# Performance work log

Measured on AMD Instinct MI355X. Metric: run time of the kernel, lower is better.

## Reference

```python
import jax, jax.numpy as jnp
import numpy as np

H = 512          # hidden_size
B, S, L = 32, 2048, 2
D = 2 * H        # encoder output / hidden feature dim


def setup_inputs() -> dict:
    key = jax.random.key(0)
    ks = jax.random.split(key, 9)
    lim1 = 1.0 / np.sqrt(D)
    limv = 1.0 / np.sqrt(H)
    return {
        "hidden": jax.random.normal(ks[0], (L, B, D), jnp.float32),
        "encoder_outputs": jax.random.normal(ks[1], (B, S, D), jnp.float32),
        "mask": jax.random.randint(ks[2], (B, S), 0, 2, jnp.int32),
        "W1_w": jax.random.uniform(ks[3], (H, D), jnp.float32, -lim1, lim1),
        "W1_b": jax.random.uniform(ks[4], (H,), jnp.float32, -lim1, lim1),
        "W2_w": jax.random.uniform(ks[5], (H, D), jnp.float32, -lim1, lim1),
        "W2_b": jax.random.uniform(ks[6], (H,), jnp.float32, -lim1, lim1),
        "V_w": jax.random.uniform(ks[7], (1, H), jnp.float32, -limv, limv),
        "V_b": jax.random.uniform(ks[8], (1,), jnp.float32, -limv, limv),
    }


def reference(hidden, encoder_outputs, mask, W1_w, W1_b, W2_w, W2_b, V_w, V_b):
    # query: last layer hidden state, broadcast over sequence -> [B, 1, D]
    query = hidden[-1][:, None, :]
    # W1(enc) + W2(query): [B, S, H]
    proj = (jnp.einsum('bsd,hd->bsh', encoder_outputs, W1_w) + W1_b
            + jnp.einsum('bqd,hd->bqh', query, W2_w) + W2_b)
    # V projection -> scores [B, S]
    score = jnp.einsum('bsh,h->bs', jnp.tanh(proj), V_w[0]) + V_b[0]
    score = jnp.where(mask == 0, jnp.float32(-1e9), score)
    attn_weights = jax.nn.softmax(score, axis=1)          # [B, S]
    context = jnp.einsum('bs,bsd->bd', attn_weights, encoder_outputs)  # [B, D]
    return context, attn_weights
```

## Files before the change

kernel.cpp:

```cpp
#include <hip/hip_runtime.h>
#include <hip/hip_bf16.h>

#define B_ 32
#define S_ 2048
#define D_ 1024
#define H_ 512
#define M_ (B_*S_)
#define BM 128
#define BN 128
#define BK 64
#define TILE (BM*BK)

typedef __attribute__((ext_vector_type(8))) short short8;
typedef __attribute__((ext_vector_type(4))) float f32x4;

__device__ __forceinline__ unsigned short f2bf(float f){
  return __builtin_bit_cast(unsigned short, __float2bfloat16(f));
}

__device__ __forceinline__ float fast_tanh(float x){
  return 1.f - 2.f*__builtin_amdgcn_rcpf(__expf(2.f*x) + 1.f);
}

__device__ __forceinline__ int swz(int row, int kshort){
  return row*BK + ((kshort & 56) ^ ((row&7)<<3)) + (kshort & 7);
}

__global__ __launch_bounds__(256) void convw_kernel(
    const float* __restrict__ W1, unsigned short* __restrict__ W1f){
  int g = blockIdx.x*256 + threadIdx.x;
  int lane = g & 63, r = g >> 6;
  int kh = r & 1, ni = (r>>1)&3, wh = (r>>3)&1, kt = (r>>4)&15, bn = r>>8;
  int h  = bn*128 + wh*64 + ni*16 + (lane&15);
  int k0 = kt*64 + kh*32 + (lane>>4)*8;
  const float* src = W1 + (size_t)h*D_ + k0;
  float4 lo = *(const float4*)src;
  float4 hi = *(const float4*)(src+4);
  short8 v;
  v[0]=(short)f2bf(lo.x); v[1]=(short)f2bf(lo.y); v[2]=(short)f2bf(lo.z); v[3]=(short)f2bf(lo.w);
  v[4]=(short)f2bf(hi.x); v[5]=(short)f2bf(hi.y); v[6]=(short)f2bf(hi.z); v[7]=(short)f2bf(hi.w);
  *(short8*)&W1f[(size_t)g*8] = v;
}

__global__ __launch_bounds__(256) void qbias_kernel(
    const float* __restrict__ hidden, const float* __restrict__ W2,
    const float* __restrict__ W1b, const float* __restrict__ W2b,
    float* __restrict__ qb){
  int b = blockIdx.x, h0 = blockIdx.y*64;
  int wave = threadIdx.x>>6, lane = threadIdx.x&63;
  const float* q = hidden + (size_t)(B_ + b)*D_;
  for (int i=0;i<16;i++){
    int h = h0 + wave*16 + i;
    const float* w = W2 + (size_t)h*D_;
    float s = 0.f;
    #pragma unroll
    for (int it=0; it<4; ++it){
      int d = it*256 + lane*4;
      const float4 qq = *(const float4*)(q+d);
      const float4 ww = *(const float4*)(w+d);
      s += qq.x*ww.x + qq.y*ww.y + qq.z*ww.z + qq.w*ww.w;
    }
    #pragma unroll
    for (int off=1; off<64; off<<=1) s += __shfl_xor(s, off);
    if (lane==0) qb[b*H_ + h] = s + W1b[h] + W2b[h];
  }
}

__global__ __launch_bounds__(256, 2) void score_gemm(
    const float* __restrict__ enc, const unsigned short* __restrict__ W1f,
    const float* __restrict__ qb, const float* __restrict__ Vw,
    float* __restrict__ score_p){
  const int id  = blockIdx.x;
  const int xcd = id & 7;
  const int j   = id >> 3;
  const int bm  = xcd*64 + (j >> 2);
  const int bn  = j & 3;
  const int m0 = bm*BM, h0 = bn*BN;
  const int tid = threadIdx.x, lane = tid&63, wave = tid>>6;
  const int wm = (wave>>1)*64, wh = wave&1, wn = wh*64;

  __shared__ __align__(16) unsigned short As[2][TILE];

  f32x4 acc[4][4];
  #pragma unroll
  for (int i=0;i<4;i++)
    #pragma unroll
    for (int j2=0;j2<4;j2++)
      acc[i][j2] = (f32x4)(0.f);

  float4 aLo[4], aHi[4];
  short8 b0[4][2], b1[4][2];

#define LOAD_A(KT) do{ const int kkx=(KT)*BK; \
  _Pragma("unroll") for (int i=0;i<4;i++){ \
    int c=tid+i*256; int row=c>>3, kc=(c&7)*8; \
    const float4* pa=(const float4*)(enc+(size_t)(m0+row)*D_+kkx+kc); \
    aLo[i]=pa[0]; aHi[i]=pa[1]; } }while(0)

#define CVT_A(P) do{ \
  _Pragma("unroll") for (int i=0;i<4;i++){ \
    int c=tid+i*256; int row=c>>3, kc=(c&7)*8; short8 av; \
    av[0]=(short)f2bf(aLo[i].x); av[1]=(short)f2bf(aLo[i].y); \
    av[2]=(short)f2bf(aLo[i].z); av[3]=(short)f2bf(aLo[i].w); \
    av[4]=(short)f2bf(aHi[i].x); av[5]=(short)f2bf(aHi[i].y); \
    av[6]=(short)f2bf(aHi[i].z); av[7]=(short)f2bf(aHi[i].w); \
    *(short8*)&As[P][swz(row,kc)] = av; } }while(0)

#define GLOB_B(KT, BB) do{ \
  const size_t sb = (size_t)(((bn*16+(KT))*2+wh)*8)*512 + lane*8; \
  _Pragma("unroll") for (int ni=0;ni<4;ni++) \
    _Pragma("unroll") for (int kh=0;kh<2;kh++) \
      BB[ni][kh] = *(const short8*)&W1f[sb + (size_t)(ni*2+kh)*512]; }while(0)

#define COMPUTE(P, BB) do{ \
  _Pragma("unroll") for (int kh=0; kh<2; ++kh){ \
    const int kb = kh*32 + (lane>>4)*8; \
    short8 af[4]; \
    _Pragma("unroll") for (int mi=0;mi<4;mi++){ \
      int row=wm+mi*16+(lane&15); af[mi]=*(const short8*)&As[P][swz(row,kb)]; } \
    _Pragma("unroll") for (int mi=0;mi<4;mi++) \
      _Pragma("unroll") for (int ni=0;ni<4;ni++) \
        acc[mi][ni]=__builtin_amdgcn_mfma_f32_16x16x32_bf16(af[mi],BB[ni][kh],acc[mi][ni],0,0,0); \
  } }while(0)

#define BODY(KT, BC, BN_) do{ \
  GLOB_B((KT)+1, BN_); \
  __builtin_amdgcn_sched_barrier(0); \
  COMPUTE((KT)&1, BC); \
  CVT_A(((KT)+1)&1); \
  LOAD_A((KT)+2); \
  asm volatile("s_waitcnt lgkmcnt(0)" ::: "memory"); \
  __builtin_amdgcn_s_barrier(); }while(0)

  LOAD_A(0);
  GLOB_B(0, b0);
  CVT_A(0);
  LOAD_A(1);
  asm volatile("s_waitcnt lgkmcnt(0)" ::: "memory");
  __builtin_amdgcn_s_barrier();

  for (int k2=0; k2<7; ++k2){
    BODY(2*k2,   b0, b1);
    BODY(2*k2+1, b1, b0);
  }
  GLOB_B(15, b1);
  __builtin_amdgcn_sched_barrier(0);
  COMPUTE(0, b0);
  CVT_A(1);
  asm volatile("s_waitcnt lgkmcnt(0)" ::: "memory");
  __builtin_amdgcn_s_barrier();
  COMPUTE(1, b1);

  const int bidx = m0 >> 11;
  float qv[4], vwv[4];
  #pragma unroll
  for (int ni=0;ni<4;ni++){
    int h = h0 + wn + ni*16 + (lane&15);
    qv[ni]  = qb[bidx*H_ + h];
    vwv[ni] = Vw[h];
  }
  __shared__ float psum[4][BM];
  #pragma unroll
  for (int mi=0;mi<4;mi++){
    #pragma unroll
    for (int r=0;r<4;r++){
      float s = 0.f;
      #pragma unroll
      for (int ni=0;ni<4;ni++) s += fast_tanh(acc[mi][ni][r] + qv[ni]) * vwv[ni];
      s += __shfl_xor(s,1); s += __shfl_xor(s,2);
      s += __shfl_xor(s,4); s += __shfl_xor(s,8);
      if ((lane&15)==0){
        int m = wm + mi*16 + ((lane>>4)<<2) + r;
        psum[wave][m] = s;
      }
    }
  }
  __syncthreads();
  if (tid < BM){
    int w0 = (tid>>6)*2;
    score_p[(size_t)bn*M_ + m0 + tid] = psum[w0][tid] + psum[w0+1][tid];
  }
}

__global__ __launch_bounds__(256) void softmax_kernel(
    const float* __restrict__ score_p, const int* __restrict__ mask,
    float* __restrict__ attn){
  int b = blockIdx.x, tid = threadIdx.x;
  int wave = tid>>6, lane = tid&63;
  __shared__ float red[8];
  float v[8];
  float mx = -1e30f;
  #pragma unroll
  for (int i=0;i<8;i++){
    int idx = b*S_ + tid + i*256;
    float sc = score_p[idx] + score_p[M_+idx] + score_p[2*M_+idx] + score_p[3*M_+idx];
    v[i] = (mask[idx]==0) ? -1e9f : sc;
    mx = fmaxf(mx, v[i]);
  }
  #pragma unroll
  for (int off=1; off<64; off<<=1) mx = fmaxf(mx, __shfl_xor(mx, off));
  if (lane==0) red[wave] = mx;
  __syncthreads();
  mx = fmaxf(fmaxf(red[0],red[1]), fmaxf(red[2],red[3]));
  float sum = 0.f;
  #pragma unroll
  for (int i=0;i<8;i++){ v[i] = __expf(v[i]-mx); sum += v[i]; }
  #pragma unroll
  for (int off=1; off<64; off<<=1) sum += __shfl_xor(sum, off);
  if (lane==0) red[4+wave] = sum;
  __syncthreads();
  float inv = 1.f/(red[4]+red[5]+red[6]+red[7]);
  #pragma unroll
  for (int i=0;i<8;i++) attn[b*S_ + tid + i*256] = v[i]*inv;
}

__global__ __launch_bounds__(256) void context_kernel(
    const float* __restrict__ enc, const float* __restrict__ attn,
    float* __restrict__ ctx){
  int b = blockIdx.x, sc = blockIdx.y;
  int s0 = sc*64;
  int d4 = threadIdx.x*4;
  const float* ep = enc + ((size_t)b*S_ + s0)*D_ + d4;
  const float* ap = attn + b*S_ + s0;
  float4 a0 = make_float4(0.f,0.f,0.f,0.f);
  float4 a1 = make_float4(0.f,0.f,0.f,0.f);
  #pragma unroll 4
  for (int i=0;i<64;i+=2){
    float w0 = ap[i], w1 = ap[i+1];
    float4 e0 = *(const float4*)(ep + (size_t)i*D_);
    float4 e1 = *(const float4*)(ep + (size_t)(i+1)*D_);
    a0.x = fmaf(w0, e0.x, a0.x); a0.y = fmaf(w0, e0.y, a0.y);
    a0.z = fmaf(w0, e0.z, a0.z); a0.w = fmaf(w0, e0.w, a0.w);
    a1.x = fmaf(w1, e1.x, a1.x); a1.y = fmaf(w1, e1.y, a1.y);
    a1.z = fmaf(w1, e1.z, a1.z); a1.w = fmaf(w1, e1.w, a1.w);
  }
  float* o = ctx + b*D_ + d4;
  atomicAdd(o+0, a0.x+a1.x); atomicAdd(o+1, a0.y+a1.y);
  atomicAdd(o+2, a0.z+a1.z); atomicAdd(o+3, a0.w+a1.w);
}

extern "C" void kernel_launch(void* const* d_in, const int* in_sizes, int n_in,
                              void* d_out, int out_size, void* d_ws, size_t ws_size,
                              hipStream_t stream){
  const float* hidden = (const float*)d_in[0];
  const float* enc    = (const float*)d_in[1];
  const int*   mask   = (const int*)d_in[2];
  const float* W1w    = (const float*)d_in[3];
  const float* W1b    = (const float*)d_in[4];
  const float* W2w    = (const float*)d_in[5];
  const float* W2b    = (const float*)d_in[6];
  const float* Vw     = (const float*)d_in[7];
  float* out = (float*)d_out;

  float* qb           = (float*)d_ws;
  float* score_p      = qb + B_*H_;
  unsigned short* W1f = (unsigned short*)(score_p + 4*M_);

  hipMemsetAsync(out, 0, (size_t)B_*D_*sizeof(float), stream);

  convw_kernel  <<<H_*D_/8/256,     256, 0, stream>>>(W1w, W1f);
  qbias_kernel  <<<dim3(B_, H_/64), 256, 0, stream>>>(hidden, W2w, W1b, W2b, qb);
  score_gemm    <<<4*(M_/BM),       256, 0, stream>>>(enc, W1f, qb, Vw, score_p);
  softmax_kernel<<<B_,              256, 0, stream>>>(score_p, mask, out + B_*D_);
  context_kernel<<<dim3(B_, 32),    256, 0, stream>>>(enc, out + B_*D_, out);
}
```

Before: 192.8 us.

## Load encoder A fragments directly from global into registers, drop LDS staging

Replaces the shared-memory double-buffered A tile (fp32 load, bf16 convert, swizzled LDS store, barrier, LDS read) with per-wave direct global loads of the exact MFMA A-fragment rows, converted to bf16 in registers. Removes LDS traffic and block barriers, and raises the occupancy hint to 3 blocks per CU. The trade-off is that the two waves sharing the same rows now each read those encoder rows from global memory, doubling A traffic through L2. The loads also come out as less coalesced strided float4 reads, with only half a K-tile of prefetch to hide latency.

```diff
diff --git a/kernel.cpp b/kernel.cpp
--- a/kernel.cpp
+++ b/kernel.cpp
@@ -9,7 +9,6 @@
 #define BM 128
 #define BN 128
 #define BK 64
-#define TILE (BM*BK)
 
 typedef __attribute__((ext_vector_type(8))) short short8;
 typedef __attribute__((ext_vector_type(4))) float f32x4;
@@ -20,10 +19,6 @@
 
 __device__ __forceinline__ float fast_tanh(float x){
   return 1.f - 2.f*__builtin_amdgcn_rcpf(__expf(2.f*x) + 1.f);
-}
-
-__device__ __forceinline__ int swz(int row, int kshort){
-  return row*BK + ((kshort & 56) ^ ((row&7)<<3)) + (kshort & 7);
 }
 
 __global__ __launch_bounds__(256) void convw_kernel(
@@ -66,7 +61,7 @@
   }
 }
 
-__global__ __launch_bounds__(256, 2) void score_gemm(
+__global__ __launch_bounds__(256, 3) void score_gemm(
     const float* __restrict__ enc, const unsigned short* __restrict__ W1f,
     const float* __restrict__ qb, const float* __restrict__ Vw,
     float* __restrict__ score_p){
@@ -79,8 +74,6 @@
   const int tid = threadIdx.x, lane = tid&63, wave = tid>>6;
   const int wm = (wave>>1)*64, wh = wave&1, wn = wh*64;
 
-  __shared__ __align__(16) unsigned short As[2][TILE];
-
   f32x4 acc[4][4];
   #pragma unroll
   for (int i=0;i<4;i++)
@@ -88,68 +81,56 @@
     for (int j2=0;j2<4;j2++)
       acc[i][j2] = (f32x4)(0.f);
 
-  float4 aLo[4], aHi[4];
-  short8 b0[4][2], b1[4][2];
-
-#define LOAD_A(KT) do{ const int kkx=(KT)*BK; \
-  _Pragma("unroll") for (int i=0;i<4;i++){ \
-    int c=tid+i*256; int row=c>>3, kc=(c&7)*8; \
-    const float4* pa=(const float4*)(enc+(size_t)(m0+row)*D_+kkx+kc); \
-    aLo[i]=pa[0]; aHi[i]=pa[1]; } }while(0)
-
-#define CVT_A(P) do{ \
-  _Pragma("unroll") for (int i=0;i<4;i++){ \
-    int c=tid+i*256; int row=c>>3, kc=(c&7)*8; short8 av; \
-    av[0]=(short)f2bf(aLo[i].x); av[1]=(short)f2bf(aLo[i].y); \
-    av[2]=(short)f2bf(aLo[i].z); av[3]=(short)f2bf(aLo[i].w); \
-    av[4]=(short)f2bf(aHi[i].x); av[5]=(short)f2bf(aHi[i].y); \
-    av[6]=(short)f2bf(aHi[i].z); av[7]=(short)f2bf(aHi[i].w); \
-    *(short8*)&As[P][swz(row,kc)] = av; } }while(0)
-
-#define GLOB_B(KT, BB) do{ \
-  const size_t sb = (size_t)(((bn*16+(KT))*2+wh)*8)*512 + lane*8; \
-  _Pragma("unroll") for (int ni=0;ni<4;ni++) \
-    _Pragma("unroll") for (int kh=0;kh<2;kh++) \
-      BB[ni][kh] = *(const short8*)&W1f[sb + (size_t)(ni*2+kh)*512]; }while(0)
-
-#define COMPUTE(P, BB) do{ \
-  _Pragma("unroll") for (int kh=0; kh<2; ++kh){ \
-    const int kb = kh*32 + (lane>>4)*8; \
-    short8 af[4]; \
-    _Pragma("unroll") for (int mi=0;mi<4;mi++){ \
-      int row=wm+mi*16+(lane&15); af[mi]=*(const short8*)&As[P][swz(row,kb)]; } \
-    _Pragma("unroll") for (int mi=0;mi<4;mi++) \
-      _Pragma("unroll") for (int ni=0;ni<4;ni++) \
-        acc[mi][ni]=__builtin_amdgcn_mfma_f32_16x16x32_bf16(af[mi],BB[ni][kh],acc[mi][ni],0,0,0); \
-  } }while(0)
-
-#define BODY(KT, BC, BN_) do{ \
-  GLOB_B((KT)+1, BN_); \
-  __builtin_amdgcn_sched_barrier(0); \
-  COMPUTE((KT)&1, BC); \
-  CVT_A(((KT)+1)&1); \
-  LOAD_A((KT)+2); \
-  asm volatile("s_waitcnt lgkmcnt(0)" ::: "memory"); \
-  __builtin_amdgcn_s_barrier(); }while(0)
-
-  LOAD_A(0);
-  GLOB_B(0, b0);
-  CVT_A(0);
-  LOAD_A(1);
-  asm volatile("s_waitcnt lgkmcnt(0)" ::: "memory");
-  __builtin_amdgcn_s_barrier();
-
-  for (int k2=0; k2<7; ++k2){
-    BODY(2*k2,   b0, b1);
-    BODY(2*k2+1, b1, b0);
-  }
-  GLOB_B(15, b1);
-  __builtin_amdgcn_sched_barrier(0);
-  COMPUTE(0, b0);
-  CVT_A(1);
-  asm volatile("s_waitcnt lgkmcnt(0)" ::: "memory");
-  __builtin_amdgcn_s_barrier();
-  COMPUTE(1, b1);
+  const float* rowp[4];
+  #pragma unroll
+  for (int mi=0;mi<4;mi++)
+    rowp[mi] = enc + (size_t)(m0 + wm + mi*16 + (lane&15))*D_ + (lane>>4)*8;
+
+  const unsigned short* bbase = W1f + (size_t)((bn*16)*2 + wh)*8*512 + lane*8;
+
+  float4 afp[4][2];
+  short8 ab[4];
+  short8 b[4][2];
+
+#define LOADA(KT,KH) do{ const int kb=(KT)*64+(KH)*32; \
+  _Pragma("unroll") for (int mi=0;mi<4;mi++){ \
+    afp[mi][0] = *(const float4*)(rowp[mi]+kb); \
+    afp[mi][1] = *(const float4*)(rowp[mi]+kb+4); } }while(0)
+
+#define CVTA() do{ \
+  _Pragma("unroll") for (int mi=0;mi<4;mi++){ \
+    short8 av; \
+    av[0]=(short)f2bf(afp[mi][0].x); av[1]=(short)f2bf(afp[mi][0].y); \
+    av[2]=(short)f2bf(afp[mi][0].z); av[3]=(short)f2bf(afp[mi][0].w); \
+    av[4]=(short)f2bf(afp[mi][1].x); av[5]=(short)f2bf(afp[mi][1].y); \
+    av[6]=(short)f2bf(afp[mi][1].z); av[7]=(short)f2bf(afp[mi][1].w); \
+    ab[mi]=av; } }while(0)
+
+  LOADA(0,0);
+
+  for (int kt=0; kt<16; ++kt){
+    const unsigned short* bp = bbase + (size_t)(kt*2)*8*512;
+    #pragma unroll
+    for (int ni=0;ni<4;ni++)
+      #pragma unroll
+      for (int kh=0;kh<2;kh++)
+        b[ni][kh] = *(const short8*)(bp + (ni*2+kh)*512);
+    CVTA();
+    LOADA(kt,1);
+    #pragma unroll
+    for (int mi=0;mi<4;mi++)
+      #pragma unroll
+      for (int ni=0;ni<4;ni++)
+        acc[mi][ni] = __builtin_amdgcn_mfma_f32_16x16x32_bf16(ab[mi], b[ni][0], acc[mi][ni], 0,0,0);
+    CVTA();
+    const int ktn = (kt<15) ? kt+1 : 15;
+    LOADA(ktn,0);
+    #pragma unroll
+    for (int mi=0;mi<4;mi++)
+      #pragma unroll
+      for (int ni=0;ni<4;ni++)
+        acc[mi][ni] = __builtin_amdgcn_mfma_f32_16x16x32_bf16(ab[mi], b[ni][1], acc[mi][ni], 0,0,0);
+  }
 
   const int bidx = m0 >> 11;
   float qv[4], vwv[4];
```

Measured after the change: 375.7 us. 94.9% more time.
